# Kernel tuning notes

Measured on AMD Instinct MI355X. Metric: run time of the kernel, lower is better.

Reference implementation:

```python
import jax, jax.numpy as jnp
import numpy as np

HEADS = 16
DIMS = [64, 64, 64, 64]  # [d_att(Q), d_att(K), d_ff(V), d_ff(G)]
EPS = 1e-4
P_POW = 2


def _cdist(Q, K):
    # Euclidean pairwise distance via the norm expansion, like torch.cdist.
    # Q: [h, b, t, d], K: [h, b, t, d] -> [h, b, t, t]
    q2 = jnp.sum(Q * Q, axis=-1)  # [h, b, t]
    k2 = jnp.sum(K * K, axis=-1)  # [h, b, t]
    qk = jnp.einsum('hbtd,hbsd->hbts', Q, K)
    d2 = q2[..., :, None] + k2[..., None, :] - 2.0 * qk
    return jnp.sqrt(jnp.maximum(d2, 0.0))


def setup_inputs() -> dict:
    key = jax.random.key(0)
    ks = jax.random.split(key, 4)
    b, t, d_in = 2, 2048, 1024
    d_proj = HEADS * sum(DIMS)  # 4096
    X = jax.random.normal(ks[0], (b, t, d_in), dtype=jnp.float32)
    W_in = jax.random.normal(ks[1], (d_in, d_proj), dtype=jnp.float32) * (d_in ** -0.5)
    b_in = jnp.zeros((d_proj,), dtype=jnp.float32)
    W_out = jax.random.normal(ks[2], (HEADS * DIMS[2], d_in), dtype=jnp.float32) * ((HEADS * DIMS[2]) ** -0.5)
    b_out = jnp.zeros((d_in,), dtype=jnp.float32)
    return {"X": X, "W_in": W_in, "b_in": b_in, "W_out": W_out, "b_out": b_out}


def reference(X, W_in, b_in, W_out, b_out):
    b, t, _ = X.shape
    # multi-head input projection: [b,t,d_in] -> [h,b,t,sum(DIMS)] -> split
    P = X @ W_in + b_in                       # [b, t, h*sum(DIMS)]
    P = P.reshape(b, t, HEADS, sum(DIMS))
    P = jnp.transpose(P, (2, 0, 1, 3))        # [h, b, t, sum(DIMS)]
    splits = np.cumsum(DIMS)[:-1]
    Q, K, V, G = jnp.split(P, splits, axis=-1)
    # Shepard's attention: inverse-power-distance weights
    W = jnp.power(EPS + _cdist(Q, K), -P_POW)         # [h, b, t, t]
    W = W / (EPS + jnp.sum(W, axis=-1, keepdims=True))
    A = jnp.einsum('hbts,hbse->hbte', W, V)           # [h, b, t, e]
    H = G * A                                          # gating
    H = jnp.transpose(H, (1, 2, 0, 3)).reshape(b, t, HEADS * DIMS[2])
    return H @ W_out + b_out
```

## Files before the change

### kernel.cpp

```cpp
#include <hip/hip_runtime.h>
#include <hip/hip_bf16.h>
#include <cstdint>
#include <cstddef>

typedef __bf16 bf16_t;
typedef __attribute__((ext_vector_type(8))) __bf16 bf16x8;
typedef __attribute__((ext_vector_type(4))) float f32x4;
typedef __attribute__((ext_vector_type(16))) float f32x16;
typedef __attribute__((ext_vector_type(4))) unsigned int u32x4;

#define ATT_EPS 1e-4f

__device__ __forceinline__ f32x4 mfma_bf16(bf16x8 a, bf16x8 b, f32x4 c) {
  return __builtin_amdgcn_mfma_f32_16x16x32_bf16(a, b, c, 0, 0, 0);
}
__device__ __forceinline__ f32x16 mfma32(bf16x8 a, bf16x8 b, f32x16 c) {
  return __builtin_amdgcn_mfma_f32_32x32x16_bf16(a, b, c, 0, 0, 0);
}
__device__ __forceinline__ unsigned cvtpk_bf16(float lo, float hi) {
  unsigned r;
  asm("v_cvt_pk_bf16_f32 %0, %1, %2" : "=v"(r) : "v"(lo), "v"(hi));
  return r;
}

#define GLDS16(g, l)                                                          \
  __builtin_amdgcn_global_load_lds(                                           \
      (const __attribute__((address_space(1))) void*)(g),                     \
      (__attribute__((address_space(3))) void*)(l), 16, 0, 0)

#define BARRAW() asm volatile("s_barrier" ::: "memory")
#define WAITV8() asm volatile("s_waitcnt vmcnt(8)" ::: "memory")
#define WAITV4() asm volatile("s_waitcnt vmcnt(4)" ::: "memory")
#define WAITV0() asm volatile("s_waitcnt vmcnt(0)" ::: "memory")

__global__ __launch_bounds__(256) void prep_kernel(
    const float* __restrict__ Wi, bf16_t* __restrict__ WiT,
    const float* __restrict__ Wo, bf16_t* __restrict__ WoT,
    const float* __restrict__ X, bf16_t* __restrict__ Xb) {
  __shared__ float T[64][65];
  if (blockIdx.y >= 20) {
    int i = ((blockIdx.y - 20) * 64 + blockIdx.x) * 256 + threadIdx.x;
    const f32x4* src = (const f32x4*)X + (size_t)i * 4;
    f32x4 a = src[0], b = src[1], c = src[2], d = src[3];
    bf16x8 o0, o1;
    o0[0] = (__bf16)a[0]; o0[1] = (__bf16)a[1]; o0[2] = (__bf16)a[2]; o0[3] = (__bf16)a[3];
    o0[4] = (__bf16)b[0]; o0[5] = (__bf16)b[1]; o0[6] = (__bf16)b[2]; o0[7] = (__bf16)b[3];
    o1[0] = (__bf16)c[0]; o1[1] = (__bf16)c[1]; o1[2] = (__bf16)c[2]; o1[3] = (__bf16)c[3];
    o1[4] = (__bf16)d[0]; o1[5] = (__bf16)d[1]; o1[6] = (__bf16)d[2]; o1[7] = (__bf16)d[3];
    ((bf16x8*)Xb)[(size_t)i * 2] = o0;
    ((bf16x8*)Xb)[(size_t)i * 2 + 1] = o1;
    return;
  }
  int tx = threadIdx.x & 63, ty = threadIdx.x >> 6;
  const float* W;
  bf16_t* Wt;
  int c0, r0, R, C;
  if (blockIdx.y < 16) {
    W = Wi; Wt = WiT; R = 1024; C = 4096;
    c0 = blockIdx.x * 64; r0 = blockIdx.y * 64;
  } else {
    int idx = (blockIdx.y - 16) * 64 + blockIdx.x;
    if (idx >= 256) return;
    W = Wo; Wt = WoT; R = 1024; C = 1024;
    c0 = (idx & 15) * 64; r0 = (idx >> 4) * 64;
  }
#pragma unroll
  for (int i = 0; i < 16; ++i) {
    int rr = ty * 16 + i;
    T[rr][tx] = W[(size_t)(r0 + rr) * C + c0 + tx];
  }
  __syncthreads();
#pragma unroll
  for (int i = 0; i < 16; ++i) {
    int cc = ty * 16 + i;
    Wt[(size_t)(c0 + cc) * R + r0 + tx] = (bf16_t)T[tx][cc];
  }
}

__global__ __launch_bounds__(512, 2) void gemm1_kernel(
    const bf16_t* __restrict__ A, const bf16_t* __restrict__ Bt,
    const float* __restrict__ bias, bf16_t* __restrict__ P,
    float* __restrict__ Q2, bf16_t* __restrict__ K2E, bf16_t* __restrict__ VtG) {
  __shared__ bf16_t As[4][2][128 * 32];
  __shared__ bf16_t Bs[4][2][128 * 32];

  const int K = 1024, N = 4096;
  int tid = threadIdx.x, lane = tid & 63, wv = tid >> 6;
  int l15 = lane & 15, lhi = lane >> 4;
  int wm = wv >> 2, wn = wv & 3;
  int swz = (blockIdx.x & 7) * 32 + (blockIdx.x >> 3);
  int tm = swz >> 4, tn = swz & 15;
  int m0 = tm << 8, n0 = tn << 8;
  int h = tn;

  int srow = tid >> 2, su = tid & 3;
  int scc = (su ^ ((srow >> 1) & 3)) << 3;
  auto stage2 = [&](int t, int pq) {
    int k0 = t * 32 + scc;
    if (pq == 0) {
      GLDS16(A + (size_t)(m0 + srow) * K + k0, &As[t & 3][0][tid * 8]);
      GLDS16(A + (size_t)(m0 + 128 + srow) * K + k0, &As[t & 3][1][tid * 8]);
    } else {
      GLDS16(Bt + (size_t)(n0 + srow) * K + k0, &Bs[t & 3][0][tid * 8]);
      GLDS16(Bt + (size_t)(n0 + 128 + srow) * K + k0, &Bs[t & 3][1][tid * 8]);
    }
  };

  f32x4 zero = {0.f, 0.f, 0.f, 0.f};
  f32x4 acc[8][4];
#pragma unroll
  for (int mf = 0; mf < 8; ++mf)
#pragma unroll
    for (int nf = 0; nf < 4; ++nf) acc[mf][nf] = zero;

  int bh = wn >> 1;
  int cidb = (wn & 1) * 64 + l15;

  stage2(0, 0); stage2(0, 1);
  stage2(1, 0); stage2(1, 1);
  stage2(2, 0); stage2(2, 1);
  WAITV8();
  BARRAW();

  for (int t = 0; t < 32; ++t) {
    int buf = t & 3;
    bf16x8 af0[4], bfr[4];
#pragma unroll
    for (int i = 0; i < 4; ++i) {
      int mfr = i * 16 + l15;
      af0[i] = *(const bf16x8*)&As[buf][wm][mfr * 32 + ((lhi ^ ((mfr >> 1) & 3)) << 3)];
    }
#pragma unroll
    for (int nf = 0; nf < 4; ++nf) {
      int cid = cidb + nf * 16;
      bfr[nf] = *(const bf16x8*)&Bs[buf][bh][cid * 32 + ((lhi ^ ((cid >> 1) & 3)) << 3)];
    }
    if (t + 3 < 32) stage2(t + 3, 0);
#pragma unroll
    for (int i = 0; i < 4; ++i)
#pragma unroll
      for (int nf = 0; nf < 4; ++nf)
        acc[i][nf] = mfma_bf16(af0[i], bfr[nf], acc[i][nf]);
    bf16x8 af1[4];
#pragma unroll
    for (int i = 0; i < 4; ++i) {
      int mfr = (4 + i) * 16 + l15;
      af1[i] = *(const bf16x8*)&As[buf][wm][mfr * 32 + ((lhi ^ ((mfr >> 1) & 3)) << 3)];
    }
    if (t + 3 < 32) stage2(t + 3, 1);
#pragma unroll
    for (int i = 0; i < 4; ++i)
#pragma unroll
      for (int nf = 0; nf < 4; ++nf)
        acc[4 + i][nf] = mfma_bf16(af1[i], bfr[nf], acc[4 + i][nf]);
    if (t <= 28) WAITV8();
    else if (t == 29) WAITV4();
    else if (t == 30) WAITV0();
    BARRAW();
  }

#pragma unroll
  for (int nf = 0; nf < 4; ++nf) {
    float bv = bias[n0 + wn * 64 + nf * 16 + l15];
#pragma unroll
    for (int mf = 0; mf < 8; ++mf)
#pragma unroll
      for (int r = 0; r < 4; ++r) acc[mf][nf][r] += bv;
  }

  if (wn != 2) {
#pragma unroll
    for (int nf = 0; nf < 4; ++nf) {
      int col = n0 + wn * 64 + nf * 16 + l15;
#pragma unroll
      for (int mf = 0; mf < 8; ++mf) {
        int rowb = m0 + wm * 128 + mf * 16 + lhi * 4;
#pragma unroll
        for (int r = 0; r < 4; ++r)
          P[(size_t)(rowb + r) * N + col] = (bf16_t)acc[mf][nf][r];
      }
    }
  }

  if (wn < 2) {
#pragma unroll
    for (int mf = 0; mf < 8; ++mf)
#pragma unroll
      for (int r = 0; r < 4; ++r) {
        float s = 0.f;
#pragma unroll
        for (int nf = 0; nf < 4; ++nf) s += acc[mf][nf][r] * acc[mf][nf][r];
        s += __shfl_xor(s, 1);
        s += __shfl_xor(s, 2);
        s += __shfl_xor(s, 4);
        s += __shfl_xor(s, 8);
        if (l15 == 0) {
          int row = m0 + wm * 128 + mf * 16 + lhi * 4 + r;
          if (wn == 0) {
            Q2[h * 4096 + row] = s;
          } else {
            __bf16 kh = (__bf16)s;
            __bf16 kl = (__bf16)(s - (float)kh);
            bf16x8 rw;
            rw[0] = kh; rw[1] = kl;
            rw[2] = (__bf16)1.f; rw[3] = (__bf16)1.f;
            rw[4] = (__bf16)0.f; rw[5] = (__bf16)0.f;
            rw[6] = (__bf16)0.f; rw[7] = (__bf16)0.f;
            *(bf16x8*)&K2E[((size_t)h * 4096 + row) * 8] = rw;
          }
        }
      }
  }

  bf16_t* T = &As[0][0][0];
  if (wn == 2) {
#pragma unroll
    for (int mf = 0; mf < 8; ++mf)
#pragma unroll
      for (int nf = 0; nf < 4; ++nf)
#pragma unroll
        for (int r = 0; r < 4; ++r) {
          int row = wm * 128 + mf * 16 + lhi * 4 + r;
          int e = nf * 16 + l15;
          int prow = (row & ~15) | ((row & 3) | ((row & 4) << 1) | ((row & 8) >> 1));
          T[e * 264 + prow] = (bf16_t)acc[mf][nf][r];
        }
  }
  __syncthreads();
  {
    int e = tid >> 3, c0 = (tid & 7) * 32;
    bf16_t* dst = VtG + (size_t)(h * 64 + e) * 4096 + m0 + c0;
#pragma unroll
    for (int j = 0; j < 4; ++j)
      *(bf16x8*)&dst[j * 8] = *(bf16x8*)&T[e * 264 + c0 + j * 8];
  }
}

template <int OUTF32>
__global__ __launch_bounds__(256, 2) void gemm_kernel(
    const bf16_t* __restrict__ A, const bf16_t* __restrict__ Bt,
    const float* __restrict__ bias, void* __restrict__ Cout,
    int M, int N, int K) {
  __shared__ bf16_t As[2][128 * 64];
  __shared__ bf16_t Bs[2][128 * 64];
  int tid = threadIdx.x, lane = tid & 63, wv = tid >> 6;
  int l15 = lane & 15, lhi = lane >> 4;
  int NT = N >> 7;
  int nwg = gridDim.x;
  int qq = nwg >> 3;
  int swz = (blockIdx.x & 7) * qq + (blockIdx.x >> 3);
  int tm = swz / NT, tn = swz % NT;
  int m0 = tm << 7, n0 = tn << 7;
  int wm = (wv >> 1) << 6, wn = (wv & 1) << 6;
  int KT = K >> 6;

  auto stage = [&](int buf, int kt) {
    int k0 = kt << 6;
#pragma unroll
    for (int s = 0; s < 4; ++s) {
      int t = s * 256 + tid;
      int row = t >> 3, u = t & 7;
      int cc = (u ^ (row & 7)) << 3;
      GLDS16(A + (size_t)(m0 + row) * K + k0 + cc, &As[buf][t * 8]);
    }
#pragma unroll
    for (int s = 0; s < 4; ++s) {
      int t = s * 256 + tid;
      int row = t >> 3, u = t & 7;
      int cc = (u ^ (row & 7)) << 3;
      GLDS16(Bt + (size_t)(n0 + row) * K + k0 + cc, &Bs[buf][t * 8]);
    }
  };

  f32x4 zero = {0.f, 0.f, 0.f, 0.f};
  f32x4 acc[4][4];
#pragma unroll
  for (int ms = 0; ms < 4; ++ms)
#pragma unroll
    for (int ns = 0; ns < 4; ++ns) acc[ms][ns] = zero;

  stage(0, 0);
  __syncthreads();
  int cur = 0;
  for (int kt = 0; kt < KT; ++kt) {
    if (kt + 1 < KT) stage(cur ^ 1, kt + 1);
#pragma unroll
    for (int ks = 0; ks < 2; ++ks) {
      bf16x8 af[4], bfr[4];
#pragma unroll
      for (int ms = 0; ms < 4; ++ms) {
        int row = wm + ms * 16 + l15;
        af[ms] = *(const bf16x8*)&As[cur][row * 64 + (((ks * 4 + lhi) ^ (row & 7)) << 3)];
      }
#pragma unroll
      for (int ns = 0; ns < 4; ++ns) {
        int col = wn + ns * 16 + l15;
        bfr[ns] = *(const bf16x8*)&Bs[cur][col * 64 + (((ks * 4 + lhi) ^ (col & 7)) << 3)];
      }
#pragma unroll
      for (int ms = 0; ms < 4; ++ms)
#pragma unroll
        for (int ns = 0; ns < 4; ++ns)
          acc[ms][ns] = mfma_bf16(af[ms], bfr[ns], acc[ms][ns]);
    }
    __syncthreads();
    cur ^= 1;
  }

#pragma unroll
  for (int ns = 0; ns < 4; ++ns) {
    int col = n0 + wn + ns * 16 + l15;
    float bv = bias[col];
#pragma unroll
    for (int ms = 0; ms < 4; ++ms) {
      int rowb = m0 + wm + ms * 16 + lhi * 4;
#pragma unroll
      for (int r = 0; r < 4; ++r) {
        float v = acc[ms][ns][r] + bv;
        if (OUTF32)
          ((float*)Cout)[(size_t)(rowb + r) * N + col] = v;
        else
          ((bf16_t*)Cout)[(size_t)(rowb + r) * N + col] = (bf16_t)v;
      }
    }
  }
}

__global__ __launch_bounds__(512, 4) void attn_kernel(
    const bf16_t* __restrict__ P, const bf16_t* __restrict__ VtG,
    const float* __restrict__ Q2, const bf16_t* __restrict__ K2E,
    bf16_t* __restrict__ H) {
  __shared__ union Smem {
    struct {
      bf16_t Ks[2][64 * 64];
      bf16_t Vts[2][64 * 64];
      bf16_t K2e[2][64 * 8];
    } l;
    float Comb[4][64][33];
  } sm;
  __shared__ float invLds[4][32];

  int tid = threadIdx.x, lane = tid & 63, wv = tid >> 6;
  int l31 = lane & 31, hi = lane >> 5, hi4 = hi * 4;
  int qw = wv & 3, sw = wv >> 2;
  int sOff = sw * 32;
  int swz = (blockIdx.x & 7) * 64 + (blockIdx.x >> 3);
  int hb = swz >> 4, qt = swz & 15;
  int h = hb >> 1, b = hb & 1;
  int rowbase = b * 2048;
  const bf16_t* Pq = P + (size_t)rowbase * 4096 + h * 256;
  const bf16_t* Pk = Pq + 64;
  const bf16_t* Pg = Pq + 192;
  const bf16_t* Vg = VtG + (size_t)h * 64 * 4096 + rowbase;
  const float* Q2g = Q2 + h * 4096 + rowbase;
  const bf16_t* K2Eg = K2E + ((size_t)h * 4096 + rowbase) * 8;
  int q0 = qt * 128 + qw * 32;

  auto stageKV = [&](int buf, int s0) {
    {
      int row = tid >> 3, u = tid & 7;
      int cc = (u ^ (row & 7)) << 3;
      GLDS16(Pk + (size_t)(s0 + row) * 4096 + cc, &sm.l.Ks[buf][tid * 8]);
    }
    {
      int row = tid >> 3, u = tid & 7;
      int cc = (u ^ (row & 7)) << 3;
      GLDS16(Vg + (size_t)row * 4096 + s0 + cc, &sm.l.Vts[buf][tid * 8]);
    }
    if (tid < 64)
      GLDS16(K2Eg + (size_t)(s0 + tid) * 8, &sm.l.K2e[buf][tid * 8]);
  };

  bf16x8 qm[4];
#pragma unroll
  for (int db = 0; db < 4; ++db) {
    bf16x8 q = *(const bf16x8*)(Pq + (size_t)(q0 + l31) * 4096 + db * 16 + hi * 8);
    u32x4 u = *(u32x4*)&q;
    u = (u ^ 0x80008000u) + 0x00800080u;
    qm[db] = *(bf16x8*)&u;
  }
  float q2s = Q2g[q0 + l31];
  __bf16 q2h = (__bf16)q2s;
  __bf16 q2l = (__bf16)(q2s - (float)q2h);
  bf16x8 qmE;
  qmE[0] = hi ? (__bf16)0.f : (__bf16)1.f;
  qmE[1] = qmE[0];
  qmE[2] = hi ? (__bf16)0.f : q2h;
  qmE[3] = hi ? (__bf16)0.f : q2l;
  qmE[4] = (__bf16)0.f; qmE[5] = (__bf16)0.f;
  qmE[6] = (__bf16)0.f; qmE[7] = (__bf16)0.f;

  f32x16 zero16;
#pragma unroll
  for (int r = 0; r < 16; ++r) zero16[r] = 0.f;

  f32x16 nacc0 = zero16, nacc1 = zero16;
  float dacc0 = 0.f, dacc1 = 0.f;

  stageKV(0, 0);
  __syncthreads();

  for (int st = 0; st < 32; ++st) {
    int cur = st & 1;
    int s0 = st * 64;
    if (st + 1 < 32) stageKV(cur ^ 1, s0 + 64);

    const bf16_t* KsC = sm.l.Ks[cur];
    const bf16_t* VtC = sm.l.Vts[cur];
    const bf16_t* K2eC = sm.l.K2e[cur];
    {
      int srow = sOff + l31;
      bf16x8 ke = *(const bf16x8*)&K2eC[srow * 8];
      u32x4 keu = *(u32x4*)&ke;
      u32x4 kz;
      kz[0] = hi ? 0u : keu[0];
      kz[1] = hi ? 0u : keu[1];
      kz[2] = 0u; kz[3] = 0u;
      bf16x8 kfE = *(bf16x8*)&kz;
      f32x16 D = mfma32(kfE, qmE, zero16);
#pragma unroll
      for (int db = 0; db < 4; ++db) {
        bf16x8 kf = *(const bf16x8*)&KsC[srow * 64 + (((db * 2 + hi) ^ (srow & 7)) << 3)];
        D = mfma32(kf, qm[db], D);
      }
      float p[16];
#pragma unroll
      for (int r = 0; r < 16; ++r) {
        float w = __builtin_amdgcn_rcpf(fmaxf(D[r], 1e-12f));
        if (r & 1) dacc1 += w; else dacc0 += w;
        p[r] = w;
      }
      u32x4 w0v = {cvtpk_bf16(p[0], p[1]), cvtpk_bf16(p[2], p[3]),
                   cvtpk_bf16(p[4], p[5]), cvtpk_bf16(p[6], p[7])};
      u32x4 w1v = {cvtpk_bf16(p[8], p[9]), cvtpk_bf16(p[10], p[11]),
                   cvtpk_bf16(p[12], p[13]), cvtpk_bf16(p[14], p[15])};
      bf16x8 pa0 = *(bf16x8*)&w0v;
      bf16x8 pa1 = *(bf16x8*)&w1v;
      int e = l31;
      int ciB = sw * 4;
      bf16x8 vb00 = *(const bf16x8*)&VtC[e * 64 + (((ciB + 0 + hi) ^ (e & 7)) << 3)];
      bf16x8 vb01 = *(const bf16x8*)&VtC[(e + 32) * 64 + (((ciB + 0 + hi) ^ ((e + 32) & 7)) << 3)];
      bf16x8 vb10 = *(const bf16x8*)&VtC[e * 64 + (((ciB + 2 + hi) ^ (e & 7)) << 3)];
      bf16x8 vb11 = *(const bf16x8*)&VtC[(e + 32) * 64 + (((ciB + 2 + hi) ^ ((e + 32) & 7)) << 3)];
      nacc0 = mfma32(pa0, vb00, nacc0);
      nacc1 = mfma32(pa0, vb01, nacc1);
      nacc0 = mfma32(pa1, vb10, nacc0);
      nacc1 = mfma32(pa1, vb11, nacc1);
    }
    __syncthreads();
  }

  if (sw == 1) {
#pragma unroll
    for (int r = 0; r < 16; ++r) {
      sm.Comb[qw][lane][r] = nacc0[r];
      sm.Comb[qw][lane][16 + r] = nacc1[r];
    }
    sm.Comb[qw][lane][32] = dacc0 + dacc1;
  }
  __syncthreads();
  if (sw == 0) {
    float dacc = dacc0 + dacc1 + sm.Comb[qw][lane][32];
#pragma unroll
    for (int r = 0; r < 16; ++r) {
      nacc0[r] += sm.Comb[qw][lane][r];
      nacc1[r] += sm.Comb[qw][lane][16 + r];
    }
    dacc += __shfl_xor(dacc, 32);
    float inv = __builtin_amdgcn_rcpf(ATT_EPS + dacc);
    if (lane < 32) invLds[qw][l31] = inv;
    __builtin_amdgcn_s_waitcnt(0);
#pragma unroll
    for (int r = 0; r < 16; ++r) {
      int q = (r & 3) + 8 * (r >> 2) + hi4;
      int tq = q0 + q;
      float iv = invLds[qw][q];
      float g0 = (float)Pg[(size_t)tq * 4096 + l31];
      float g1 = (float)Pg[(size_t)tq * 4096 + 32 + l31];
      H[(size_t)(rowbase + tq) * 1024 + h * 64 + l31] = (bf16_t)(g0 * nacc0[r] * iv);
      H[(size_t)(rowbase + tq) * 1024 + h * 64 + 32 + l31] = (bf16_t)(g1 * nacc1[r] * iv);
    }
  }
}

extern "C" void kernel_launch(void* const* d_in, const int* in_sizes, int n_in,
                              void* d_out, int out_size, void* d_ws, size_t ws_size,
                              hipStream_t stream) {
  const float* X     = (const float*)d_in[0];
  const float* W_in  = (const float*)d_in[1];
  const float* b_in  = (const float*)d_in[2];
  const float* W_out = (const float*)d_in[3];
  const float* b_out = (const float*)d_in[4];

  char* ws = (char*)d_ws;
  bf16_t* Xb  = (bf16_t*)(ws);
  bf16_t* WbT = (bf16_t*)(ws + ((size_t)8  << 20));
  bf16_t* WoT = (bf16_t*)(ws + ((size_t)16 << 20));
  bf16_t* Pb  = (bf16_t*)(ws + ((size_t)18 << 20));
  bf16_t* Hb  = (bf16_t*)(ws + ((size_t)50 << 20));
  float*  Q2  = (float*) (ws + ((size_t)58 << 20));
  bf16_t* VtG = (bf16_t*)d_out;
  bf16_t* K2E = (bf16_t*)((char*)d_out + ((size_t)8 << 20));

  prep_kernel<<<dim3(64, 36), 256, 0, stream>>>(W_in, WbT, W_out, WoT, X, Xb);
  gemm1_kernel<<<256, 512, 0, stream>>>(Xb, WbT, b_in, Pb, Q2, K2E, VtG);
  attn_kernel<<<512, 512, 0, stream>>>(Pb, VtG, Q2, K2E, Hb);
  gemm_kernel<1><<<256, 256, 0, stream>>>(Hb, WoT, b_out, d_out, 4096, 1024, 1024);
}
```

Before: 127.4 us.

## Deepen attention K/V staging to four-buffer pipeline with per-wave vmcnt waits

The attention kernel moves from a double-buffered K/V/K2e LDS ring to a four-slot ring that keeps three tiles in flight. The per-iteration __syncthreads is replaced by explicit vmcnt waits sized to each wave's outstanding loads (wave 0 also issues the K2e loads) plus a raw barrier. The aim is to hide global-to-LDS latency better, at the cost of roughly doubled LDS use. To fit that, the occupancy hint drops from 4 to 2 blocks per CU.

```diff
diff --git a/kernel.cpp b/kernel.cpp
--- a/kernel.cpp
+++ b/kernel.cpp
@@ -29,9 +29,7 @@
       (__attribute__((address_space(3))) void*)(l), 16, 0, 0)
 
 #define BARRAW() asm volatile("s_barrier" ::: "memory")
-#define WAITV8() asm volatile("s_waitcnt vmcnt(8)" ::: "memory")
-#define WAITV4() asm volatile("s_waitcnt vmcnt(4)" ::: "memory")
-#define WAITV0() asm volatile("s_waitcnt vmcnt(0)" ::: "memory")
+#define WAITVN(n) asm volatile("s_waitcnt vmcnt(" #n ")" ::: "memory")
 
 __global__ __launch_bounds__(256) void prep_kernel(
     const float* __restrict__ Wi, bf16_t* __restrict__ WiT,
@@ -119,7 +117,7 @@
   stage2(0, 0); stage2(0, 1);
   stage2(1, 0); stage2(1, 1);
   stage2(2, 0); stage2(2, 1);
-  WAITV8();
+  WAITVN(8);
   BARRAW();
 
   for (int t = 0; t < 32; ++t) {
@@ -153,9 +151,9 @@
 #pragma unroll
       for (int nf = 0; nf < 4; ++nf)
         acc[4 + i][nf] = mfma_bf16(af1[i], bfr[nf], acc[4 + i][nf]);
-    if (t <= 28) WAITV8();
-    else if (t == 29) WAITV4();
-    else if (t == 30) WAITV0();
+    if (t <= 28) WAITVN(8);
+    else if (t == 29) WAITVN(4);
+    else if (t == 30) WAITVN(0);
     BARRAW();
   }
 
@@ -326,15 +324,15 @@
   }
 }
 
-__global__ __launch_bounds__(512, 4) void attn_kernel(
+__global__ __launch_bounds__(512, 2) void attn_kernel(
     const bf16_t* __restrict__ P, const bf16_t* __restrict__ VtG,
     const float* __restrict__ Q2, const bf16_t* __restrict__ K2E,
     bf16_t* __restrict__ H) {
   __shared__ union Smem {
     struct {
-      bf16_t Ks[2][64 * 64];
-      bf16_t Vts[2][64 * 64];
-      bf16_t K2e[2][64 * 8];
+      bf16_t Ks[4][64 * 64];
+      bf16_t Vts[4][64 * 64];
+      bf16_t K2e[4][64 * 8];
     } l;
     float Comb[4][64][33];
   } sm;
@@ -355,6 +353,7 @@
   const float* Q2g = Q2 + h * 4096 + rowbase;
   const bf16_t* K2Eg = K2E + ((size_t)h * 4096 + rowbase) * 8;
   int q0 = qt * 128 + qw * 32;
+  bool w0 = (wv == 0);
 
   auto stageKV = [&](int buf, int s0) {
     {
@@ -398,16 +397,19 @@
   float dacc0 = 0.f, dacc1 = 0.f;
 
   stageKV(0, 0);
-  __syncthreads();
+  stageKV(1, 64);
+  stageKV(2, 128);
+  if (w0) WAITVN(6); else WAITVN(4);
+  BARRAW();
 
   for (int st = 0; st < 32; ++st) {
-    int cur = st & 1;
+    int buf = st & 3;
     int s0 = st * 64;
-    if (st + 1 < 32) stageKV(cur ^ 1, s0 + 64);
-
-    const bf16_t* KsC = sm.l.Ks[cur];
-    const bf16_t* VtC = sm.l.Vts[cur];
-    const bf16_t* K2eC = sm.l.K2e[cur];
+    if (st + 3 < 32) stageKV((st + 3) & 3, s0 + 192);
+
+    const bf16_t* KsC = sm.l.Ks[buf];
+    const bf16_t* VtC = sm.l.Vts[buf];
+    const bf16_t* K2eC = sm.l.K2e[buf];
     {
       int srow = sOff + l31;
       bf16x8 ke = *(const bf16x8*)&K2eC[srow * 8];
@@ -447,7 +449,10 @@
       nacc0 = mfma32(pa1, vb10, nacc0);
       nacc1 = mfma32(pa1, vb11, nacc1);
     }
-    __syncthreads();
+    if (st <= 28) { if (w0) WAITVN(6); else WAITVN(4); }
+    else if (st == 29) { if (w0) WAITVN(3); else WAITVN(2); }
+    else if (st == 30) WAITVN(0);
+    BARRAW();
   }
 
   if (sw == 1) {
```

After: 128.4 us. About the same (+0.8%).
